# Kernel tuning notes

Measured on AMD Instinct MI355X. Metric: run time of the kernel, lower is better.

The kernel has to match this reference:

```python
import jax, jax.numpy as jnp
import numpy as np

E = 1024        # embed_dim
NH = 16         # num_heads
HD = E // NH    # head_dim = 64
MLP = 4096
HID = int(2 * MLP / 3)  # 2730, TransNeXt ConvGLU hidden
NT = 1          # no_rope task tokens (skip rotary / skip dwconv)
B, S = 8, 1025
GRID = 32       # sqrt(S - NT)
EPS = 1e-6
SCALE = HD ** -0.5


def rmsnorm(x, g):
    return x * jax.lax.rsqrt(jnp.mean(x * x, axis=-1, keepdims=True) + EPS) * g


def apply_rope(t):
    # t: [B, NH, s, HD] -- rotate-half RoPE over image-token positions
    s = t.shape[2]
    pos = jnp.arange(s, dtype=jnp.float32)
    inv_freq = 1.0 / (10000.0 ** (jnp.arange(0, HD, 2, dtype=jnp.float32) / HD))
    freqs = pos[:, None] * inv_freq[None, :]          # [s, HD/2]
    cos = jnp.concatenate([jnp.cos(freqs)] * 2, -1)   # [s, HD]
    sin = jnp.concatenate([jnp.sin(freqs)] * 2, -1)
    t1, t2 = jnp.split(t, 2, axis=-1)
    rot = jnp.concatenate([-t2, t1], axis=-1)
    return t * cos + rot * sin


def rope_skip_task(t):
    # first NT tokens are task tokens -> identity; rest get rotary with positions 0..
    return jnp.concatenate([t[:, :, :NT], apply_rope(t[:, :, NT:])], axis=2)


def setup_inputs() -> dict:
    key = jax.random.key(0)
    ks = jax.random.split(key, 12)
    init = lambda k, shape, fan: (jax.random.normal(k, shape, jnp.float32) * (fan ** -0.5))
    return {
        "x": jax.random.normal(ks[0], (B, S, E), jnp.float32),
        "g1": jnp.ones((E,), jnp.float32),
        "w_qkv": init(ks[1], (E, 3 * E), E),
        "b_qkv": jnp.zeros((3 * E,), jnp.float32),
        "w_proj": init(ks[2], (E, E), E),
        "b_proj": jnp.zeros((E,), jnp.float32),
        "g2": jnp.ones((E,), jnp.float32),
        "fc1_w": init(ks[3], (E, 2 * HID), E),
        "fc1_b": jnp.zeros((2 * HID,), jnp.float32),
        "dw_w": init(ks[4], (3, 3, 1, HID), 9),  # HWIO depthwise 3x3
        "dw_b": jnp.zeros((HID,), jnp.float32),
        "fc2_w": init(ks[5], (HID, E), HID),
        "fc2_b": jnp.zeros((E,), jnp.float32),
    }


def reference(x, g1, w_qkv, b_qkv, w_proj, b_proj, g2, fc1_w, fc1_b, dw_w, dw_b, fc2_w, fc2_b):
    # ---- attention block ----
    residual = x
    xn = rmsnorm(x, g1)
    qkv = xn @ w_qkv + b_qkv                              # [B,S,3E]
    qkv = qkv.reshape(B, S, 3, NH, HD).transpose(2, 0, 3, 1, 4)
    q, k, v = qkv[0], qkv[1], qkv[2]                      # [B,NH,S,HD]
    q = rope_skip_task(q)
    k = rope_skip_task(k)
    attn = jnp.einsum("bhqd,bhkd->bhqk", q * SCALE, k)    # [B,NH,S,S]
    attn = jax.nn.softmax(attn, axis=-1)
    out = jnp.einsum("bhqk,bhkd->bhqd", attn, v)          # [B,NH,S,HD]
    out = out.transpose(0, 2, 1, 3).reshape(B, S, E)
    out = out @ w_proj + b_proj
    x = residual + out

    # ---- ConvGLU MLP block ----
    residual = x
    xn = rmsnorm(x, g2)
    h = xn @ fc1_w + fc1_b                                # [B,S,2*HID]
    xg, vg = jnp.split(h, 2, axis=-1)
    x_task, x_img = xg[:, :NT], xg[:, NT:]                # dwconv only on image tokens
    img = x_img.reshape(B, GRID, GRID, HID)
    img = jax.lax.conv_general_dilated(
        img, dw_w, window_strides=(1, 1), padding="SAME",
        feature_group_count=HID,
        dimension_numbers=("NHWC", "HWIO", "NHWC")) + dw_b
    x_img = img.reshape(B, GRID * GRID, HID)
    xc = jnp.concatenate([x_task, x_img], axis=1)
    h = jax.nn.gelu(xc, approximate=False) * vg           # GLU gate
    h = h @ fc2_w + fc2_b
    return residual + h
```

## Files before the change

### kernel.cpp

```cpp
#include <hip/hip_runtime.h>
#include <hip/hip_bf16.h>
#include <math.h>

#define E_DIM 1024
#define NHEAD 16
#define HID_DIM 2730
#define KP_FC2 2752
#define HB_LD 5504
#define B_DIM 8
#define S_DIM 1025
#define EPS_V 1e-6f
#define SCALE_V 0.125f
#define MROWS (B_DIM * S_DIM)

typedef __attribute__((ext_vector_type(8))) short short8;
typedef __attribute__((ext_vector_type(4))) float f32x4;
typedef unsigned short us;

__device__ __forceinline__ float b2f(us u) {
    union { unsigned int i; float f; } x; x.i = ((unsigned int)u) << 16; return x.f;
}
__device__ __forceinline__ us f2b(float f) {
    __hip_bfloat16 h = __float2bfloat16(f);
    return *reinterpret_cast<us*>(&h);
}

__device__ __forceinline__ void stage16(const void* g, void* l) {
    __builtin_amdgcn_global_load_lds(
        (const __attribute__((address_space(1))) unsigned int*)g,
        (__attribute__((address_space(3))) unsigned int*)l,
        16, 0, 0);
}

__device__ __forceinline__ int sl(int row, int c8) {
    return (row * 8 + (c8 ^ (row & 7))) * 8;
}

#define MFMA16(a, b, c) __builtin_amdgcn_mfma_f32_16x16x32_bf16(a, b, c, 0, 0, 0)

__global__ __launch_bounds__(256) void rmsnorm_kernel(const float* __restrict__ x,
        const float* __restrict__ g, us* __restrict__ out) {
    int row = blockIdx.x;
    const float4* xr = (const float4*)(x + (size_t)row * E_DIM);
    float4 v = xr[threadIdx.x];
    float ss = v.x*v.x + v.y*v.y + v.z*v.z + v.w*v.w;
    #pragma unroll
    for (int off = 32; off > 0; off >>= 1) ss += __shfl_down(ss, off, 64);
    __shared__ float wsum[4];
    int lane = threadIdx.x & 63, w = threadIdx.x >> 6;
    if (lane == 0) wsum[w] = ss;
    __syncthreads();
    float tot = wsum[0] + wsum[1] + wsum[2] + wsum[3];
    float inv = rsqrtf(tot * (1.0f / E_DIM) + EPS_V);
    float4 gv = ((const float4*)g)[threadIdx.x];
    ushort4 o;
    o.x = f2b(v.x * inv * gv.x); o.y = f2b(v.y * inv * gv.y);
    o.z = f2b(v.z * inv * gv.z); o.w = f2b(v.w * inv * gv.w);
    ((ushort4*)(out + (size_t)row * E_DIM))[threadIdx.x] = o;
}

__global__ __launch_bounds__(256) void convt_kernel(const float* __restrict__ W,
        us* __restrict__ WT, int K, int N, int KPad, int swap_half) {
    __shared__ float T[32][33];
    int n0 = blockIdx.x * 32, k0 = blockIdx.y * 32;
    int c = threadIdx.x & 31, r4 = (threadIdx.x >> 5) << 2;
    #pragma unroll
    for (int i = 0; i < 4; i++) {
        int k = k0 + r4 + i, n = n0 + c;
        int src = n;
        if (swap_half && n < N) src = (n < swap_half) ? n + swap_half : n - swap_half;
        T[c][r4 + i] = (k < K && n < N) ? W[(size_t)k * N + src] : 0.0f;
    }
    __syncthreads();
    #pragma unroll
    for (int i = 0; i < 4; i++) {
        int n = n0 + r4 + i, k = k0 + c;
        if (n < N && k < KPad) WT[(size_t)n * KPad + k] = f2b(T[r4 + i][c]);
    }
}

__global__ __launch_bounds__(256) void bias_perm_kernel(const float* __restrict__ b,
        float* __restrict__ bp) {
    int r = blockIdx.x * 256 + threadIdx.x;
    if (r < 2 * HID_DIM) bp[r] = b[r < HID_DIM ? r + HID_DIM : r - HID_DIM];
}

template<bool BF16OUT>
__global__ __launch_bounds__(512, 2) void gemm256(const us* __restrict__ A, int lda,
        const us* __restrict__ Bt, int ldb, const float* __restrict__ bias,
        const float* __restrict__ Rres, void* __restrict__ Cv,
        int M, int N, int K, int ldc) {
    __shared__ __align__(16) us lds[2][4][8192];
    us* const L = &lds[0][0][0];
    const int tid = threadIdx.x;
    const int lane = tid & 63;
    const int w = tid >> 6;
    const int wm = w >> 2, wn = w & 3;
    const int l15 = lane & 15, quad = lane >> 4;
    const int m0 = blockIdx.y * 256, n0 = blockIdx.x * 256;

    const int r0 = tid >> 3;
    const int c80 = (tid & 7) ^ (r0 & 7);
    const us* const pA = A + (size_t)(m0 + r0) * lda + c80 * 8;
    const us* const pB = Bt + (size_t)(n0 + r0) * ldb + c80 * 8;
    const size_t a64 = (size_t)64 * lda, b64 = (size_t)64 * ldb;
    us* const dst = L + tid * 8;

#define STG_A(b, h, kt) do { \
    const us* s_ = pA + (size_t)(h) * 2 * a64 + (size_t)(kt) * 64; \
    stage16(s_,       dst + ((b) * 4 + (h)) * 8192); \
    stage16(s_ + a64, dst + ((b) * 4 + (h)) * 8192 + 4096); \
} while (0)
#define STG_B(b, h, kt) do { \
    const us* s_ = pB + (size_t)(h) * 2 * b64 + (size_t)(kt) * 64; \
    stage16(s_,       dst + ((b) * 4 + 2 + (h)) * 8192); \
    stage16(s_ + b64, dst + ((b) * 4 + 2 + (h)) * 8192 + 4096); \
} while (0)

    f32x4 acc[8][4];
    #pragma unroll
    for (int m = 0; m < 8; m++)
        #pragma unroll
        for (int n = 0; n < 4; n++) acc[m][n] = (f32x4){0.f, 0.f, 0.f, 0.f};

    const int nk = K >> 6;

    STG_A(0, 0, 0); STG_A(0, 1, 0);
    STG_B(0, 0, 0); STG_B(0, 1, 0);
    STG_B(1, 0, 1); STG_B(1, 1, 1);
    asm volatile("s_waitcnt vmcnt(4)" ::: "memory");
    __builtin_amdgcn_s_barrier();

    const int brow = (wn & 1) * 64;
    for (int t = 0; t < nk; t++) {
        const int c = t & 1, cn = c ^ 1;
        const us* aB = L + (c * 4 + wm) * 8192;
        const us* bB = L + (c * 4 + 2 + (wn >> 1)) * 8192;
        short8 bf[4][2];
        #pragma unroll
        for (int n = 0; n < 4; n++) {
            bf[n][0] = *(const short8*)(bB + sl(brow + n * 16 + l15, quad));
            bf[n][1] = *(const short8*)(bB + sl(brow + n * 16 + l15, 4 + quad));
        }
        #pragma unroll
        for (int p = 0; p < 4; p++) {
            const int mp = 2 * p;
            short8 a00 = *(const short8*)(aB + sl(mp * 16 + l15, quad));
            short8 a01 = *(const short8*)(aB + sl(mp * 16 + l15, 4 + quad));
            short8 a10 = *(const short8*)(aB + sl(mp * 16 + 16 + l15, quad));
            short8 a11 = *(const short8*)(aB + sl(mp * 16 + 16 + l15, 4 + quad));
            if (p == 0) {
                if (t + 1 < nk) { STG_A(cn, 0, t + 1); STG_A(cn, 1, t + 1); }
            } else if (p == 1) {
                if (t + 2 < nk) STG_B(c, 0, t + 2);
            } else if (p == 2) {
                if (t + 2 < nk) STG_B(c, 1, t + 2);
            }
            __builtin_amdgcn_s_barrier();
            __builtin_amdgcn_s_setprio(1);
            #pragma unroll
            for (int n = 0; n < 4; n++) {
                acc[mp][n]     = MFMA16(a00, bf[n][0], acc[mp][n]);
                acc[mp][n]     = MFMA16(a01, bf[n][1], acc[mp][n]);
                acc[mp + 1][n] = MFMA16(a10, bf[n][0], acc[mp + 1][n]);
                acc[mp + 1][n] = MFMA16(a11, bf[n][1], acc[mp + 1][n]);
            }
            __builtin_amdgcn_s_setprio(0);
            if (p == 3) {
                if (t + 2 >= nk) { asm volatile("s_waitcnt vmcnt(0)" ::: "memory"); }
                else             { asm volatile("s_waitcnt vmcnt(4)" ::: "memory"); }
            }
            __builtin_amdgcn_s_barrier();
        }
    }

    #pragma unroll
    for (int m = 0; m < 8; m++) {
        int gm0 = m0 + wm * 128 + m * 16 + quad * 4;
        #pragma unroll
        for (int n = 0; n < 4; n++) {
            int gn = n0 + wn * 64 + n * 16 + l15;
            if (gn >= N) continue;
            float bs = bias[gn];
            #pragma unroll
            for (int r = 0; r < 4; r++) {
                int gm = gm0 + r;
                if (gm >= M) continue;
                float v = acc[m][n][r] + bs;
                if (BF16OUT) {
                    ((us*)Cv)[(size_t)gm * ldc + gn] = f2b(v);
                } else {
                    ((float*)Cv)[(size_t)gm * ldc + gn] = v + Rres[(size_t)gm * ldc + gn];
                }
            }
        }
    }
#undef STG_A
#undef STG_B
}

__global__ __launch_bounds__(256) void rope_kernel(us* __restrict__ qkv) {
    int idx = blockIdx.x * 256 + threadIdx.x;
    int i = idx & 31;
    int h = (idx >> 5) & (NHEAD - 1);
    int rc = idx >> 9;
    int s = rc % S_DIM;
    us* q = qkv + (size_t)rc * 3072 + h * 64;
    us* k = q + 1024;
    if (s == 0) {
        q[i] = f2b(b2f(q[i]) * SCALE_V);
        q[i + 32] = f2b(b2f(q[i + 32]) * SCALE_V);
        return;
    }
    float pos = (float)(s - 1);
    float invf = expf((float)i * (-9.210340371976184f / 32.0f));
    float f = pos * invf;
    float c = cosf(f), sn = sinf(f);
    float q1 = b2f(q[i]), q2 = b2f(q[i + 32]);
    q[i]      = f2b((q1 * c - q2 * sn) * SCALE_V);
    q[i + 32] = f2b((q2 * c + q1 * sn) * SCALE_V);
    float k1 = b2f(k[i]), k2 = b2f(k[i + 32]);
    k[i]      = f2b(k1 * c - k2 * sn);
    k[i + 32] = f2b(k2 * c + k1 * sn);
}

__global__ __launch_bounds__(256) void vtrans_kernel(const us* __restrict__ qkv,
        us* __restrict__ Vt) {
    __shared__ us T[64][65];
    int st = blockIdx.x, h = blockIdx.y, bc = blockIdx.z;
    int tid = threadIdx.x;
    int r = tid & 63, cb = (tid >> 6) * 16;
    const us* src = qkv + (size_t)(bc * S_DIM + st * 64 + r) * 3072 + 2048 + h * 64 + cb;
    #pragma unroll
    for (int i = 0; i < 4; i++) {
        ushort4 v = *(const ushort4*)(src + i * 4);
        T[cb + i*4 + 0][r] = v.x; T[cb + i*4 + 1][r] = v.y;
        T[cb + i*4 + 2][r] = v.z; T[cb + i*4 + 3][r] = v.w;
    }
    __syncthreads();
    int d = tid >> 2, sc = (tid & 3) * 16;
    us* dstp = Vt + ((size_t)((bc * 16 + h) * 64 + d)) * 1088 + st * 64 + sc;
    #pragma unroll
    for (int g = 0; g < 4; g++) {
        ushort4 o;
        int i0 = sc + g * 4;
        o.x = (st*64 + i0 + 0 < S_DIM) ? T[d][i0 + 0] : 0;
        o.y = (st*64 + i0 + 1 < S_DIM) ? T[d][i0 + 1] : 0;
        o.z = (st*64 + i0 + 2 < S_DIM) ? T[d][i0 + 2] : 0;
        o.w = (st*64 + i0 + 3 < S_DIM) ? T[d][i0 + 3] : 0;
        *(ushort4*)(dstp + g * 4) = o;
    }
}

__global__ __launch_bounds__(256) void attn_kernel(const us* __restrict__ qkv,
        const us* __restrict__ Vt, us* __restrict__ attnb) {
    __shared__ __align__(16) us Kb[2][4096];
    __shared__ __align__(16) us Vb[2][4096];
    __shared__ __align__(16) us Ps[4096];
    int qt = blockIdx.x, h = blockIdx.y, bc = blockIdx.z;
    int tid = threadIdx.x;
    int lane = tid & 63, w = tid >> 6;
    int l15 = lane & 15, quad = lane >> 4;

    const us* qrow = qkv + (size_t)(bc * S_DIM + qt * 64 + 16 * w + l15) * 3072 + h * 64;
    short8 qa0 = *(const short8*)(qrow + quad * 8);
    short8 qa1 = *(const short8*)(qrow + 32 + quad * 8);

    const us* kg = qkv + (size_t)(bc * S_DIM) * 3072 + 1024 + h * 64;
    const us* vgp = Vt + (size_t)((bc * 16 + h) * 64) * 1088;

    int s0 = tid, s1 = 256 + tid;
    int row0 = s0 >> 3, c8_0 = (s0 & 7) ^ (row0 & 7);
    int row1 = s1 >> 3, c8_1 = (s1 & 7) ^ (row1 & 7);

    f32x4 acc_o[4];
    float mr[4], lr[4];
    #pragma unroll
    for (int r = 0; r < 4; r++) { mr[r] = -1e30f; lr[r] = 0.f; }
    #pragma unroll
    for (int j = 0; j < 4; j++) acc_o[j] = (f32x4){0.f, 0.f, 0.f, 0.f};

    stage16(kg + (size_t)row0 * 3072 + c8_0 * 8, Kb[0] + s0 * 8);
    stage16(vgp + (size_t)row0 * 1088 + c8_0 * 8, Vb[0] + s0 * 8);
    stage16(kg + (size_t)row1 * 3072 + c8_1 * 8, Kb[0] + (s1 & 255) * 8 + 2048 * 8 * 0 + 256 * 8);
    stage16(vgp + (size_t)row1 * 1088 + c8_1 * 8, Vb[0] + s1 * 8);
    __syncthreads();

    for (int kt = 0; kt < 17; kt++) {
        int cur = kt & 1, nxt = cur ^ 1;
        if (kt + 1 < 17) {
            stage16(kg + (size_t)((kt + 1) * 64 + row0) * 3072 + c8_0 * 8, Kb[nxt] + s0 * 8);
            stage16(vgp + (size_t)row0 * 1088 + (kt + 1) * 64 + c8_0 * 8, Vb[nxt] + s0 * 8);
            stage16(kg + (size_t)((kt + 1) * 64 + row1) * 3072 + c8_1 * 8, Kb[nxt] + s1 * 8);
            stage16(vgp + (size_t)row1 * 1088 + (kt + 1) * 64 + c8_1 * 8, Vb[nxt] + s1 * 8);
        }

        f32x4 accS[4];
        #pragma unroll
        for (int j = 0; j < 4; j++) accS[j] = (f32x4){0.f, 0.f, 0.f, 0.f};
        __builtin_amdgcn_s_setprio(1);
        #pragma unroll
        for (int j = 0; j < 4; j++) {
            short8 kb0 = *(const short8*)(Kb[cur] + sl(16 * j + l15, quad));
            short8 kb1 = *(const short8*)(Kb[cur] + sl(16 * j + l15, 4 + quad));
            accS[j] = MFMA16(qa0, kb0, accS[j]);
            accS[j] = MFMA16(qa1, kb1, accS[j]);
        }
        __builtin_amdgcn_s_setprio(0);

        #pragma unroll
        for (int j = 0; j < 4; j++) {
            if (kt * 64 + 16 * j + l15 >= S_DIM) {
                #pragma unroll
                for (int r = 0; r < 4; r++) accS[j][r] = -1e30f;
            }
        }

        float tm[4];
        #pragma unroll
        for (int r = 0; r < 4; r++) {
            float t = fmaxf(fmaxf(accS[0][r], accS[1][r]), fmaxf(accS[2][r], accS[3][r]));
            #pragma unroll
            for (int off = 1; off < 16; off <<= 1)
                t = fmaxf(t, __shfl_xor(t, off, 64));
            tm[r] = t;
        }
        int need = (tm[0] > mr[0] + 8.f) || (tm[1] > mr[1] + 8.f) ||
                   (tm[2] > mr[2] + 8.f) || (tm[3] > mr[3] + 8.f);
        if (__any(need)) {
            #pragma unroll
            for (int r = 0; r < 4; r++) {
                float mnew = fmaxf(mr[r], tm[r]);
                float al = __expf(mr[r] - mnew);
                mr[r] = mnew;
                lr[r] *= al;
                #pragma unroll
                for (int j = 0; j < 4; j++) acc_o[j][r] *= al;
            }
        }
        float pr[4][4];
        #pragma unroll
        for (int r = 0; r < 4; r++) {
            float rs = 0.f;
            #pragma unroll
            for (int j = 0; j < 4; j++) {
                float p = __expf(accS[j][r] - mr[r]);
                pr[j][r] = p;
                rs += p;
            }
            lr[r] += rs;
        }
        #pragma unroll
        for (int j = 0; j < 4; j++) {
            #pragma unroll
            for (int r = 0; r < 4; r++) {
                int prow = quad * 4 + r;
                int idx = sl(16 * w + prow, 2 * j + (l15 >> 3)) + (l15 & 7);
                Ps[idx] = f2b(pr[j][r]);
            }
        }
        short8 pa0 = *(const short8*)(Ps + sl(16 * w + l15, quad));
        short8 pa1 = *(const short8*)(Ps + sl(16 * w + l15, 4 + quad));
        __builtin_amdgcn_s_setprio(1);
        #pragma unroll
        for (int j = 0; j < 4; j++) {
            short8 vb0 = *(const short8*)(Vb[cur] + sl(16 * j + l15, quad));
            short8 vb1 = *(const short8*)(Vb[cur] + sl(16 * j + l15, 4 + quad));
            acc_o[j] = MFMA16(pa0, vb0, acc_o[j]);
            acc_o[j] = MFMA16(pa1, vb1, acc_o[j]);
        }
        __builtin_amdgcn_s_setprio(0);
        __syncthreads();
    }

    #pragma unroll
    for (int r = 0; r < 4; r++) {
        #pragma unroll
        for (int off = 1; off < 16; off <<= 1)
            lr[r] += __shfl_xor(lr[r], off, 64);
    }
    #pragma unroll
    for (int r = 0; r < 4; r++) {
        int s = qt * 64 + 16 * w + quad * 4 + r;
        if (s >= S_DIM) continue;
        float invl = 1.0f / lr[r];
        #pragma unroll
        for (int j = 0; j < 4; j++)
            attnb[(size_t)(bc * S_DIM + s) * E_DIM + h * 64 + 16 * j + l15] =
                f2b(acc_o[j][r] * invl);
    }
}

__global__ __launch_bounds__(256) void conv_gelu_kernel(us* __restrict__ hb,
        const float* __restrict__ dw_w, const float* __restrict__ dw_b) {
    int p = blockIdx.x % S_DIM;
    size_t row = blockIdx.x;
    size_t brow = row - p;
    for (int c = threadIdx.x; c < HID_DIM; c += 256) {
        float val;
        if (p == 0) {
            val = b2f(hb[row * HB_LD + HID_DIM + c]);
        } else {
            int pp = p - 1;
            int gy = pp >> 5, gx = pp & 31;
            float a = dw_b[c];
            #pragma unroll
            for (int dy = 0; dy < 3; dy++) {
                int ny = gy + dy - 1;
                if (ny < 0 || ny >= 32) continue;
                #pragma unroll
                for (int dx = 0; dx < 3; dx++) {
                    int nx = gx + dx - 1;
                    if (nx < 0 || nx >= 32) continue;
                    a = fmaf(b2f(hb[(brow + 1 + ny * 32 + nx) * HB_LD + HID_DIM + c]),
                             dw_w[(dy * 3 + dx) * HID_DIM + c], a);
                }
            }
            val = a;
        }
        float ge = 0.5f * val * (1.0f + erff(val * 0.70710678118654752f));
        hb[row * HB_LD + c] = f2b(ge * b2f(hb[row * HB_LD + c]));
    }
}

static size_t ws_need(int cb) {
    size_t R = (size_t)cb * 1025, Rp = ((R + 127) / 128) * 128;
    size_t end1 = Rp*1024*2 + Rp*3072*2 + (size_t)cb*16*64*1088*2
                + 8320ull*1024*2 + 3072ull*1024*2 + 1024ull*1024*2;
    size_t end2 = Rp*1024*2 + Rp*HB_LD*2 + 5504ull*1024*2 + 1024ull*KP_FC2*2 + 5460*4;
    return end1 > end2 ? end1 : end2;
}

extern "C" void kernel_launch(void* const* d_in, const int* in_sizes, int n_in,
                              void* d_out, int out_size, void* d_ws, size_t ws_size,
                              hipStream_t stream) {
    const float* x      = (const float*)d_in[0];
    const float* g1     = (const float*)d_in[1];
    const float* w_qkv  = (const float*)d_in[2];
    const float* b_qkv  = (const float*)d_in[3];
    const float* w_proj = (const float*)d_in[4];
    const float* b_proj = (const float*)d_in[5];
    const float* g2     = (const float*)d_in[6];
    const float* fc1_w  = (const float*)d_in[7];
    const float* fc1_b  = (const float*)d_in[8];
    const float* dw_w   = (const float*)d_in[9];
    const float* dw_b   = (const float*)d_in[10];
    const float* fc2_w  = (const float*)d_in[11];
    const float* fc2_b  = (const float*)d_in[12];
    float* out = (float*)d_out;
    char* base = (char*)d_ws;

    int CB = 2;
    if (ws_size >= ws_need(8)) CB = 8;
    else if (ws_size >= ws_need(4)) CB = 4;
    int NC = B_DIM / CB;
    size_t R = (size_t)CB * 1025, Rp = ((R + 127) / 128) * 128;
    int gy256 = (int)((R + 255) / 256);

    us* xn    = (us*)base;
    size_t o  = Rp * 1024 * 2;
    us* qkv   = (us*)(base + o);
    us* hbuf  = (us*)(base + o);
    size_t o2 = o + Rp * 3072 * 2;
    us* Vt    = (us*)(base + o2);
    size_t o3 = o2 + (size_t)CB * 16 * 64 * 1088 * 2;
    us* attnb = (us*)(base + o3);
    size_t o4 = o3 + 8320ull * 1024 * 2;
    us* qkvT  = (us*)(base + o4);
    size_t o5 = o4 + 3072ull * 1024 * 2;
    us* projT = (us*)(base + o5);
    size_t p2 = o + Rp * HB_LD * 2;
    us* fc1T  = (us*)(base + p2);
    size_t p3 = p2 + 5504ull * 1024 * 2;
    us* fc2T  = (us*)(base + p3);
    float* fc1bp = (float*)(base + p3 + 1024ull * KP_FC2 * 2);

    convt_kernel<<<dim3(96, 32), 256, 0, stream>>>(w_qkv, qkvT, 1024, 3072, 1024, 0);
    convt_kernel<<<dim3(32, 32), 256, 0, stream>>>(w_proj, projT, 1024, 1024, 1024, 0);
    for (int c = 0; c < NC; c++) {
        size_t roff = (size_t)c * R;
        rmsnorm_kernel<<<(int)R, 256, 0, stream>>>(x + roff * E_DIM, g1, xn);
        gemm256<true><<<dim3(12, gy256), 512, 0, stream>>>(xn, 1024, qkvT, 1024,
                b_qkv, nullptr, qkv, (int)R, 3072, 1024, 3072);
        rope_kernel<<<(int)(2 * R), 256, 0, stream>>>(qkv);
        vtrans_kernel<<<dim3(17, 16, CB), 256, 0, stream>>>(qkv, Vt);
        attn_kernel<<<dim3(17, 16, CB), 256, 0, stream>>>(qkv, Vt, attnb + roff * E_DIM);
    }
    gemm256<false><<<dim3(4, (MROWS + 255) / 256), 512, 0, stream>>>(attnb, 1024,
            projT, 1024, b_proj, x, out, MROWS, 1024, 1024, 1024);

    convt_kernel<<<dim3(171, 32), 256, 0, stream>>>(fc1_w, fc1T, 1024, 5460, 1024, HID_DIM);
    convt_kernel<<<dim3(32, 86), 256, 0, stream>>>(fc2_w, fc2T, HID_DIM, 1024, KP_FC2, 0);
    bias_perm_kernel<<<22, 256, 0, stream>>>(fc1_b, fc1bp);
    for (int c = 0; c < NC; c++) {
        size_t roff = (size_t)c * R;
        float* outc = out + roff * E_DIM;
        rmsnorm_kernel<<<(int)R, 256, 0, stream>>>(outc, g2, xn);
        gemm256<true><<<dim3(22, gy256), 512, 0, stream>>>(xn, 1024, fc1T, 1024,
                fc1bp, nullptr, hbuf, (int)R, 5460, 1024, HB_LD);
        conv_gelu_kernel<<<(int)R, 256, 0, stream>>>(hbuf, dw_w, dw_b);
        gemm256<false><<<dim3(4, gy256), 512, 0, stream>>>(hbuf, HB_LD, fc2T, KP_FC2,
                fc2_b, outc, outc, (int)R, 1024, KP_FC2, 1024);
    }
}
```

Baseline: 841.2 us.

## Add XCD-aware block remap, split-K fc2 with atomics, vectorized conv-GELU, deeper B prefetch

Remaps workgroup IDs so neighbouring tiles land on the same XCD for better L2 reuse. The GEMM now prefetches the next tile's A operand earlier and carries half of the B fragments across iterations. The fc2 GEMM is split across two K halves with atomic accumulation into the residual output, which raises the small grid's parallelism. The fc1 output layout pads the xg half to an aligned offset so the conv-GELU kernel can use 8-wide vector loads. The changes also fix a K staging address in attention and add extra waitcnt and sched_barrier handling, at the cost of atomic traffic and nondeterministic summation order in fc2.

```diff
diff --git a/kernel.cpp b/kernel.cpp
--- a/kernel.cpp
+++ b/kernel.cpp
@@ -7,6 +7,8 @@
 #define HID_DIM 2730
 #define KP_FC2 2752
 #define HB_LD 5504
+#define XG_OFF 2752
+#define FC1_N 5482
 #define B_DIM 8
 #define S_DIM 1025
 #define EPS_V 1e-6f
@@ -60,16 +62,25 @@
 }
 
 __global__ __launch_bounds__(256) void convt_kernel(const float* __restrict__ W,
-        us* __restrict__ WT, int K, int N, int KPad, int swap_half) {
+        us* __restrict__ WT, int K, int N, int KPad, int swap_half, int xg_off, int Wld) {
     __shared__ float T[32][33];
     int n0 = blockIdx.x * 32, k0 = blockIdx.y * 32;
     int c = threadIdx.x & 31, r4 = (threadIdx.x >> 5) << 2;
     #pragma unroll
     for (int i = 0; i < 4; i++) {
         int k = k0 + r4 + i, n = n0 + c;
-        int src = n;
-        if (swap_half && n < N) src = (n < swap_half) ? n + swap_half : n - swap_half;
-        T[c][r4 + i] = (k < K && n < N) ? W[(size_t)k * N + src] : 0.0f;
+        float v = 0.0f;
+        if (k < K && n < N) {
+            int src = n;
+            int ok = 1;
+            if (swap_half) {
+                if (n < swap_half) src = n + swap_half;
+                else if (xg_off) { if (n >= xg_off) src = n - xg_off; else ok = 0; }
+                else src = n - swap_half;
+            }
+            if (ok) v = W[(size_t)k * Wld + src];
+        }
+        T[c][r4 + i] = v;
     }
     __syncthreads();
     #pragma unroll
@@ -82,14 +93,15 @@
 __global__ __launch_bounds__(256) void bias_perm_kernel(const float* __restrict__ b,
         float* __restrict__ bp) {
     int r = blockIdx.x * 256 + threadIdx.x;
-    if (r < 2 * HID_DIM) bp[r] = b[r < HID_DIM ? r + HID_DIM : r - HID_DIM];
-}
-
-template<bool BF16OUT>
+    if (r < FC1_N)
+        bp[r] = (r < HID_DIM) ? b[r + HID_DIM] : ((r < XG_OFF) ? 0.0f : b[r - XG_OFF]);
+}
+
+template<int MODE>
 __global__ __launch_bounds__(512, 2) void gemm256(const us* __restrict__ A, int lda,
         const us* __restrict__ Bt, int ldb, const float* __restrict__ bias,
         const float* __restrict__ Rres, void* __restrict__ Cv,
-        int M, int N, int K, int ldc) {
+        int M, int N, int K, int ldc, int Ksplit) {
     __shared__ __align__(16) us lds[2][4][8192];
     us* const L = &lds[0][0][0];
     const int tid = threadIdx.x;
@@ -97,12 +109,22 @@
     const int w = tid >> 6;
     const int wm = w >> 2, wn = w & 3;
     const int l15 = lane & 15, quad = lane >> 4;
-    const int m0 = blockIdx.y * 256, n0 = blockIdx.x * 256;
+
+    const int nwg = gridDim.x * gridDim.y;
+    const int orig = blockIdx.y * gridDim.x + blockIdx.x;
+    const int q8 = nwg >> 3, r8 = nwg & 7;
+    const int xcd = orig & 7, oi = orig >> 3;
+    const int wgid = (xcd < r8 ? xcd * (q8 + 1) : r8 * (q8 + 1) + (xcd - r8) * q8) + oi;
+    const int m0 = (wgid / gridDim.x) * 256, n0 = (wgid % gridDim.x) * 256;
+
+    const int kz = (MODE == 2) ? (int)blockIdx.z : 0;
+    const int kofs = kz * Ksplit;
+    const int Keff = (MODE == 2) ? (kz ? K - Ksplit : Ksplit) : K;
 
     const int r0 = tid >> 3;
     const int c80 = (tid & 7) ^ (r0 & 7);
-    const us* const pA = A + (size_t)(m0 + r0) * lda + c80 * 8;
-    const us* const pB = Bt + (size_t)(n0 + r0) * ldb + c80 * 8;
+    const us* const pA = A + (size_t)(m0 + r0) * lda + kofs + c80 * 8;
+    const us* const pB = Bt + (size_t)(n0 + r0) * ldb + kofs + c80 * 8;
     const size_t a64 = (size_t)64 * lda, b64 = (size_t)64 * ldb;
     us* const dst = L + tid * 8;
 
@@ -123,24 +145,41 @@
         #pragma unroll
         for (int n = 0; n < 4; n++) acc[m][n] = (f32x4){0.f, 0.f, 0.f, 0.f};
 
-    const int nk = K >> 6;
+    const int nk = Keff >> 6;
+    const int brow = (wn & 1) * 64;
 
     STG_A(0, 0, 0); STG_A(0, 1, 0);
     STG_B(0, 0, 0); STG_B(0, 1, 0);
-    STG_B(1, 0, 1); STG_B(1, 1, 1);
-    asm volatile("s_waitcnt vmcnt(4)" ::: "memory");
+    if (nk > 1) {
+        STG_B(1, 0, 1); STG_B(1, 1, 1);
+        STG_A(1, 0, 1); STG_A(1, 1, 1);
+        asm volatile("s_waitcnt vmcnt(8)" ::: "memory");
+    } else {
+        asm volatile("s_waitcnt vmcnt(0)" ::: "memory");
+    }
     __builtin_amdgcn_s_barrier();
-
-    const int brow = (wn & 1) * 64;
+    __builtin_amdgcn_sched_barrier(0);
+
+    short8 bf01[2][2];
+    {
+        const us* bB0 = L + (2 + (wn >> 1)) * 8192;
+        #pragma unroll
+        for (int n = 0; n < 2; n++) {
+            bf01[n][0] = *(const short8*)(bB0 + sl(brow + n * 16 + l15, quad));
+            bf01[n][1] = *(const short8*)(bB0 + sl(brow + n * 16 + l15, 4 + quad));
+        }
+    }
+
     for (int t = 0; t < nk; t++) {
         const int c = t & 1, cn = c ^ 1;
         const us* aB = L + (c * 4 + wm) * 8192;
         const us* bB = L + (c * 4 + 2 + (wn >> 1)) * 8192;
-        short8 bf[4][2];
-        #pragma unroll
-        for (int n = 0; n < 4; n++) {
-            bf[n][0] = *(const short8*)(bB + sl(brow + n * 16 + l15, quad));
-            bf[n][1] = *(const short8*)(bB + sl(brow + n * 16 + l15, 4 + quad));
+        const us* bBn = L + (cn * 4 + 2 + (wn >> 1)) * 8192;
+        short8 bf2[2][2];
+        #pragma unroll
+        for (int n = 0; n < 2; n++) {
+            bf2[n][0] = *(const short8*)(bB + sl(brow + (n + 2) * 16 + l15, quad));
+            bf2[n][1] = *(const short8*)(bB + sl(brow + (n + 2) * 16 + l15, 4 + quad));
         }
         #pragma unroll
         for (int p = 0; p < 4; p++) {
@@ -149,28 +188,37 @@
             short8 a01 = *(const short8*)(aB + sl(mp * 16 + l15, 4 + quad));
             short8 a10 = *(const short8*)(aB + sl(mp * 16 + 16 + l15, quad));
             short8 a11 = *(const short8*)(aB + sl(mp * 16 + 16 + l15, 4 + quad));
-            if (p == 0) {
-                if (t + 1 < nk) { STG_A(cn, 0, t + 1); STG_A(cn, 1, t + 1); }
-            } else if (p == 1) {
-                if (t + 2 < nk) STG_B(c, 0, t + 2);
-            } else if (p == 2) {
-                if (t + 2 < nk) STG_B(c, 1, t + 2);
+            if (p == 1) { if (t + 2 < nk) STG_B(c, 0, t + 2); }
+            else if (p == 2) { if (t + 2 < nk) STG_B(c, 1, t + 2); }
+            else if (p == 3) {
+                if (t + 2 < nk)      { asm volatile("s_waitcnt vmcnt(4)" ::: "memory"); }
+                else if (t + 1 < nk) { asm volatile("s_waitcnt vmcnt(0)" ::: "memory"); }
             }
             __builtin_amdgcn_s_barrier();
+            if (p == 3) __builtin_amdgcn_sched_barrier(0);
             __builtin_amdgcn_s_setprio(1);
             #pragma unroll
             for (int n = 0; n < 4; n++) {
-                acc[mp][n]     = MFMA16(a00, bf[n][0], acc[mp][n]);
-                acc[mp][n]     = MFMA16(a01, bf[n][1], acc[mp][n]);
-                acc[mp + 1][n] = MFMA16(a10, bf[n][0], acc[mp + 1][n]);
-                acc[mp + 1][n] = MFMA16(a11, bf[n][1], acc[mp + 1][n]);
+                const short8 b0 = (n < 2) ? bf01[n][0] : bf2[n - 2][0];
+                const short8 b1 = (n < 2) ? bf01[n][1] : bf2[n - 2][1];
+                acc[mp][n]     = MFMA16(a00, b0, acc[mp][n]);
+                acc[mp][n]     = MFMA16(a01, b1, acc[mp][n]);
+                acc[mp + 1][n] = MFMA16(a10, b0, acc[mp + 1][n]);
+                acc[mp + 1][n] = MFMA16(a11, b1, acc[mp + 1][n]);
             }
             __builtin_amdgcn_s_setprio(0);
             if (p == 3) {
-                if (t + 2 >= nk) { asm volatile("s_waitcnt vmcnt(0)" ::: "memory"); }
-                else             { asm volatile("s_waitcnt vmcnt(4)" ::: "memory"); }
+                if (t + 2 < nk) { STG_A(c, 0, t + 2); STG_A(c, 1, t + 2); }
+                if (t + 1 < nk) {
+                    #pragma unroll
+                    for (int n = 0; n < 2; n++) {
+                        bf01[n][0] = *(const short8*)(bBn + sl(brow + n * 16 + l15, quad));
+                        bf01[n][1] = *(const short8*)(bBn + sl(brow + n * 16 + l15, 4 + quad));
+                    }
+                }
             }
             __builtin_amdgcn_s_barrier();
+            if (p == 3) __builtin_amdgcn_sched_barrier(0);
         }
     }
 
@@ -181,16 +229,18 @@
         for (int n = 0; n < 4; n++) {
             int gn = n0 + wn * 64 + n * 16 + l15;
             if (gn >= N) continue;
-            float bs = bias[gn];
+            float bs = (MODE == 2) ? (kz == 0 ? bias[gn] : 0.0f) : bias[gn];
             #pragma unroll
             for (int r = 0; r < 4; r++) {
                 int gm = gm0 + r;
                 if (gm >= M) continue;
                 float v = acc[m][n][r] + bs;
-                if (BF16OUT) {
+                if (MODE == 0) {
                     ((us*)Cv)[(size_t)gm * ldc + gn] = f2b(v);
+                } else if (MODE == 1) {
+                    ((float*)Cv)[(size_t)gm * ldc + gn] = v + Rres[(size_t)gm * ldc + gn];
                 } else {
-                    ((float*)Cv)[(size_t)gm * ldc + gn] = v + Rres[(size_t)gm * ldc + gn];
+                    atomicAdd(&((float*)Cv)[(size_t)gm * ldc + gn], v);
                 }
             }
         }
@@ -282,7 +332,7 @@
 
     stage16(kg + (size_t)row0 * 3072 + c8_0 * 8, Kb[0] + s0 * 8);
     stage16(vgp + (size_t)row0 * 1088 + c8_0 * 8, Vb[0] + s0 * 8);
-    stage16(kg + (size_t)row1 * 3072 + c8_1 * 8, Kb[0] + (s1 & 255) * 8 + 2048 * 8 * 0 + 256 * 8);
+    stage16(kg + (size_t)row1 * 3072 + c8_1 * 8, Kb[0] + s1 * 8);
     stage16(vgp + (size_t)row1 * 1088 + c8_1 * 8, Vb[0] + s1 * 8);
     __syncthreads();
 
@@ -396,30 +446,78 @@
     int p = blockIdx.x % S_DIM;
     size_t row = blockIdx.x;
     size_t brow = row - p;
-    for (int c = threadIdx.x; c < HID_DIM; c += 256) {
-        float val;
-        if (p == 0) {
-            val = b2f(hb[row * HB_LD + HID_DIM + c]);
+    int pp = p - 1;
+    int gy = pp >> 5, gx = pp & 31;
+    for (int g = threadIdx.x; g < 342; g += 256) {
+        int c0 = g * 8;
+        if (c0 + 8 <= HID_DIM) {
+            float val[8];
+            if (p == 0) {
+                short8 xv = *(const short8*)(hb + row * HB_LD + XG_OFF + c0);
+                #pragma unroll
+                for (int e = 0; e < 8; e++) val[e] = b2f((us)xv[e]);
+            } else {
+                #pragma unroll
+                for (int e = 0; e < 8; e++) val[e] = dw_b[c0 + e];
+                #pragma unroll
+                for (int dy = 0; dy < 3; dy++) {
+                    int ny = gy + dy - 1;
+                    if (ny < 0 || ny >= 32) continue;
+                    #pragma unroll
+                    for (int dx = 0; dx < 3; dx++) {
+                        int nx = gx + dx - 1;
+                        if (nx < 0 || nx >= 32) continue;
+                        short8 xv = *(const short8*)(hb +
+                                (brow + 1 + ny * 32 + nx) * HB_LD + XG_OFF + c0);
+                        const float* wp = dw_w + (dy * 3 + dx) * HID_DIM + c0;
+                        float2 w0 = *(const float2*)(wp);
+                        float2 w1 = *(const float2*)(wp + 2);
+                        float2 w2 = *(const float2*)(wp + 4);
+                        float2 w3 = *(const float2*)(wp + 6);
+                        val[0] = fmaf(b2f((us)xv[0]), w0.x, val[0]);
+                        val[1] = fmaf(b2f((us)xv[1]), w0.y, val[1]);
+                        val[2] = fmaf(b2f((us)xv[2]), w1.x, val[2]);
+                        val[3] = fmaf(b2f((us)xv[3]), w1.y, val[3]);
+                        val[4] = fmaf(b2f((us)xv[4]), w2.x, val[4]);
+                        val[5] = fmaf(b2f((us)xv[5]), w2.y, val[5]);
+                        val[6] = fmaf(b2f((us)xv[6]), w3.x, val[6]);
+                        val[7] = fmaf(b2f((us)xv[7]), w3.y, val[7]);
+                    }
+                }
+            }
+            short8 gv = *(const short8*)(hb + row * HB_LD + c0);
+            short8 o;
+            #pragma unroll
+            for (int e = 0; e < 8; e++) {
+                float ge = 0.5f * val[e] * (1.0f + erff(val[e] * 0.70710678118654752f));
+                o[e] = (short)f2b(ge * b2f((us)gv[e]));
+            }
+            *(short8*)(hb + row * HB_LD + c0) = o;
         } else {
-            int pp = p - 1;
-            int gy = pp >> 5, gx = pp & 31;
-            float a = dw_b[c];
-            #pragma unroll
-            for (int dy = 0; dy < 3; dy++) {
-                int ny = gy + dy - 1;
-                if (ny < 0 || ny >= 32) continue;
-                #pragma unroll
-                for (int dx = 0; dx < 3; dx++) {
-                    int nx = gx + dx - 1;
-                    if (nx < 0 || nx >= 32) continue;
-                    a = fmaf(b2f(hb[(brow + 1 + ny * 32 + nx) * HB_LD + HID_DIM + c]),
-                             dw_w[(dy * 3 + dx) * HID_DIM + c], a);
+            for (int c = c0; c < HID_DIM; c++) {
+                float val;
+                if (p == 0) {
+                    val = b2f(hb[row * HB_LD + XG_OFF + c]);
+                } else {
+                    float a = dw_b[c];
+                    #pragma unroll
+                    for (int dy = 0; dy < 3; dy++) {
+                        int ny = gy + dy - 1;
+                        if (ny < 0 || ny >= 32) continue;
+                        #pragma unroll
+                        for (int dx = 0; dx < 3; dx++) {
+                            int nx = gx + dx - 1;
+                            if (nx < 0 || nx >= 32) continue;
+                            a = fmaf(b2f(hb[(brow + 1 + ny * 32 + nx) * HB_LD + XG_OFF + c]),
+                                     dw_w[(dy * 3 + dx) * HID_DIM + c], a);
+                        }
+                    }
+                    val = a;
                 }
-            }
-            val = a;
-        }
-        float ge = 0.5f * val * (1.0f + erff(val * 0.70710678118654752f));
-        hb[row * HB_LD + c] = f2b(ge * b2f(hb[row * HB_LD + c]));
+                float ge = 0.5f * val * (1.0f + erff(val * 0.70710678118654752f));
+                hb[row * HB_LD + c] = f2b(ge * b2f(hb[row * HB_LD + c]));
+            }
+        }
     }
 }
 
@@ -427,7 +525,7 @@
     size_t R = (size_t)cb * 1025, Rp = ((R + 127) / 128) * 128;
     size_t end1 = Rp*1024*2 + Rp*3072*2 + (size_t)cb*16*64*1088*2
                 + 8320ull*1024*2 + 3072ull*1024*2 + 1024ull*1024*2;
-    size_t end2 = Rp*1024*2 + Rp*HB_LD*2 + 5504ull*1024*2 + 1024ull*KP_FC2*2 + 5460*4;
+    size_t end2 = Rp*1024*2 + Rp*HB_LD*2 + 5504ull*1024*2 + 1024ull*KP_FC2*2 + 5504*4;
     return end1 > end2 ? end1 : end2;
 }
 
@@ -475,31 +573,33 @@
     us* fc2T  = (us*)(base + p3);
     float* fc1bp = (float*)(base + p3 + 1024ull * KP_FC2 * 2);
 
-    convt_kernel<<<dim3(96, 32), 256, 0, stream>>>(w_qkv, qkvT, 1024, 3072, 1024, 0);
-    convt_kernel<<<dim3(32, 32), 256, 0, stream>>>(w_proj, projT, 1024, 1024, 1024, 0);
+    convt_kernel<<<dim3(96, 32), 256, 0, stream>>>(w_qkv, qkvT, 1024, 3072, 1024, 0, 0, 3072);
+    convt_kernel<<<dim3(32, 32), 256, 0, stream>>>(w_proj, projT, 1024, 1024, 1024, 0, 0, 1024);
     for (int c = 0; c < NC; c++) {
         size_t roff = (size_t)c * R;
         rmsnorm_kernel<<<(int)R, 256, 0, stream>>>(x + roff * E_DIM, g1, xn);
-        gemm256<true><<<dim3(12, gy256), 512, 0, stream>>>(xn, 1024, qkvT, 1024,
-                b_qkv, nullptr, qkv, (int)R, 3072, 1024, 3072);
+        gemm256<0><<<dim3(12, gy256), 512, 0, stream>>>(xn, 1024, qkvT, 1024,
+                b_qkv, nullptr, qkv, (int)R, 3072, 1024, 3072, 0);
         rope_kernel<<<(int)(2 * R), 256, 0, stream>>>(qkv);
         vtrans_kernel<<<dim3(17, 16, CB), 256, 0, stream>>>(qkv, Vt);
         attn_kernel<<<dim3(17, 16, CB), 256, 0, stream>>>(qkv, Vt, attnb + roff * E_DIM);
     }
-    gemm256<false><<<dim3(4, (MROWS + 255) / 256), 512, 0, stream>>>(attnb, 1024,
-            projT, 1024, b_proj, x, out, MROWS, 1024, 1024, 1024);
-
-    convt_kernel<<<dim3(171, 32), 256, 0, stream>>>(fc1_w, fc1T, 1024, 5460, 1024, HID_DIM);
-    convt_kernel<<<dim3(32, 86), 256, 0, stream>>>(fc2_w, fc2T, HID_DIM, 1024, KP_FC2, 0);
+    gemm256<1><<<dim3(4, (MROWS + 255) / 256), 512, 0, stream>>>(attnb, 1024,
+            projT, 1024, b_proj, x, out, MROWS, 1024, 1024, 1024, 0);
+
+    convt_kernel<<<dim3(172, 32), 256, 0, stream>>>(fc1_w, fc1T, 1024, FC1_N, 1024,
+            HID_DIM, XG_OFF, 5460);
+    convt_kernel<<<dim3(32, 86), 256, 0, stream>>>(fc2_w, fc2T, HID_DIM, 1024, KP_FC2,
+            0, 0, 1024);
     bias_perm_kernel<<<22, 256, 0, stream>>>(fc1_b, fc1bp);
     for (int c = 0; c < NC; c++) {
         size_t roff = (size_t)c * R;
         float* outc = out + roff * E_DIM;
         rmsnorm_kernel<<<(int)R, 256, 0, stream>>>(outc, g2, xn);
-        gemm256<true><<<dim3(22, gy256), 512, 0, stream>>>(xn, 1024, fc1T, 1024,
-                fc1bp, nullptr, hbuf, (int)R, 5460, 1024, HB_LD);
+        gemm256<0><<<dim3(22, gy256), 512, 0, stream>>>(xn, 1024, fc1T, 1024,
+                fc1bp, nullptr, hbuf, (int)R, FC1_N, 1024, HB_LD, 0);
         conv_gelu_kernel<<<(int)R, 256, 0, stream>>>(hbuf, dw_w, dw_b);
-        gemm256<false><<<dim3(4, gy256), 512, 0, stream>>>(hbuf, HB_LD, fc2T, KP_FC2,
-                fc2_b, outc, outc, (int)R, 1024, KP_FC2, 1024);
-    }
-}
+        gemm256<2><<<dim3(4, gy256, 2), 512, 0, stream>>>(hbuf, HB_LD, fc2T, KP_FC2,
+                fc2_b, nullptr, outc, (int)R, 1024, KP_FC2, 1024, 1408);
+    }
+}
```

Result: faster. 814.0 us (-3.2%).
